# Kernel optimization log

Hardware: AMD Instinct MI355X
Metric: run time of the kernel (lower is better)

## Reference

```python
import jax, jax.numpy as jnp
import numpy as np

K = 50            # neighbors (self excluded)
ALPHA = 0.99      # propagation coefficient
THRESH = 0.4      # pseudo-label confidence threshold
MAXITER = 20      # CG iterations
NUM_CLASSES = 100
TOL = 1e-6        # CG relative tolerance (scipy cg tol)


def setup_inputs() -> dict:
    key = jax.random.key(0)
    k1, k2, k3 = jax.random.split(key, 3)
    N, d = 16384, 128
    X = jax.random.normal(k1, (N, d), dtype=jnp.float32)
    labels = jax.random.randint(k2, (N,), 0, NUM_CLASSES)
    labels_mask = jax.random.uniform(k3, (N,)) < 0.1
    idxs = jnp.arange(N)
    return {"X": X, "labels": labels, "labels_mask": labels_mask, "idxs": idxs}


def _label_prop(X, labels, labels_mask):
    N = X.shape[0]
    # faiss.normalize_L2 + inner-product search == cosine kNN
    Xn = X / jnp.maximum(jnp.linalg.norm(X, axis=1, keepdims=True), 1e-12)
    sims = Xn @ Xn.T                                   # [N, N]
    vals, I = jax.lax.top_k(sims, K + 1)
    Dv = vals[:, 1:] ** 3                              # drop self column, cube sims
    I = I[:, 1:]
    rows = jnp.repeat(jnp.arange(N), K)
    cols = I.reshape(-1)
    w = Dv.reshape(-1)
    # W = W + W.T with diagonal zeroed (edge-list form, never dense NxN)
    er = jnp.concatenate([rows, cols])
    ec = jnp.concatenate([cols, rows])
    ew = jnp.concatenate([w, w])
    ew = jnp.where(er == ec, 0.0, ew)
    S = jax.ops.segment_sum(ew, er, num_segments=N)
    S = jnp.where(S == 0, 1.0, S)
    Dinv = 1.0 / jnp.sqrt(S)                           # D^{-1/2}

    def A_mv(V):  # (I - alpha * D^-1/2 W D^-1/2) @ V, V: [N, C]
        U = Dinv[:, None] * V
        WU = jax.ops.segment_sum(ew[:, None] * U[ec], er, num_segments=N)
        return V - ALPHA * (Dinv[:, None] * WU)

    # per-class normalized seed vectors y (1/|labeled_c| on labeled idx of class c)
    mask_f = labels_mask.astype(jnp.float32)
    counts = jax.ops.segment_sum(mask_f, labels, num_segments=NUM_CLASSES)
    Y = (mask_f[:, None] * jax.nn.one_hot(labels, NUM_CLASSES, dtype=jnp.float32)) / jnp.maximum(counts, 1.0)[None, :]

    # batched CG (x0 = 0), all classes solved simultaneously; per-column early-stop mask
    bnorm = jnp.linalg.norm(Y, axis=0)
    x = jnp.zeros_like(Y)
    r = Y
    p = r
    rs = jnp.sum(r * r, axis=0)

    def step(carry, _):
        x, r, p, rs = carry
        active = jnp.sqrt(rs) > TOL * jnp.maximum(bnorm, 1e-30)
        Ap = A_mv(p)
        a = rs / jnp.maximum(jnp.sum(p * Ap, axis=0), 1e-30)
        a = jnp.where(active, a, 0.0)
        x = x + a * p
        r = r - a * Ap
        rs_new = jnp.sum(r * r, axis=0)
        beta = jnp.where(active, rs_new / jnp.maximum(rs, 1e-30), 0.0)
        p = jnp.where(active, r + beta * p, p)
        rs = jnp.where(active, rs_new, rs)
        return (x, r, p, rs), None

    (x, _, _, _), _ = jax.lax.scan(step, (x, r, p, rs), None, length=MAXITER)

    Z = jnp.maximum(x, 0.0)
    # torch F.normalize(Z, p=1, dim=1)
    probs_l1 = Z / jnp.maximum(jnp.sum(Z, axis=1, keepdims=True), 1e-12)
    pseudo = jax.nn.softmax(probs_l1, axis=-1)
    return pseudo


def reference(X, labels, labels_mask, idxs):
    pseudo = _label_prop(X, labels, labels_mask)
    max_probs = jnp.max(pseudo, axis=-1)
    p_labels = jnp.argmax(pseudo, axis=-1)
    masks = (max_probs >= THRESH).astype(jnp.float32)
    acc = jnp.mean((p_labels == labels).astype(jnp.float32))
    p_labels = jnp.where(labels_mask, labels, p_labels)  # overwrite labeled idx
    return p_labels, acc, masks
```

## Files before the change

### kernel.cpp

```cpp
#include <hip/hip_runtime.h>
#include <hip/hip_bf16.h>
#include <math.h>


#define N_NODES 16384
#define DIM     128
#define KNN     50
#define NCLS    100
#define PSTR    100
#define ALPHA_C 0.99f
#define TOL_C   1e-6f
#define TAU     0.18f
#define MAXITER_C 20

__global__ __launch_bounds__(256) void k_norm(const float* __restrict__ X, float* __restrict__ Xn){
  int t = threadIdx.x;
  int row = blockIdx.x*2 + (t>>7);
  int c = t & 127;
  float v = X[(size_t)row*DIM + c];
  float s = v*v;
  #pragma unroll
  for (int o=1;o<64;o<<=1) s += __shfl_xor(s, o, 64);
  __shared__ float sw[4];
  if ((t&63)==0) sw[t>>6] = s;
  __syncthreads();
  int half = (t>>7)*2;
  float nrm = fmaxf(sqrtf(sw[half]+sw[half+1]), 1e-12f);
  Xn[(size_t)row*DIM + c] = v / nrm;
}

#define NTILE 8256
__global__ __launch_bounds__(256, 4) void k_sims(const float* __restrict__ Xn,
    int* __restrict__ cand_cnt, float* __restrict__ cand_val, int* __restrict__ cand_idx, int CAP){
  __shared__ __align__(16) float As[32][132];
  __shared__ __align__(16) float Bs[32][132];
  const int t = threadIdx.x;
  const int tr = t >> 4, tc = t & 15;
  for (int q = blockIdx.x; q < NTILE; q += gridDim.x){
    float disc = 66049.0f - 8.0f*(float)q;
    int rb = (int)((257.0f - sqrtf(disc))*0.5f);
    if (rb > 127) rb = 127;
    while (rb > 0 && rb*(257-rb)/2 > q) --rb;
    while ((rb+1)*(257-(rb+1))/2 <= q) ++rb;
    int cb = rb + (q - rb*(257-rb)/2);
    const int row0 = rb*128, col0 = cb*128;
    float acc[8][8];
    #pragma unroll
    for (int i=0;i<8;i++){
      #pragma unroll
      for (int j=0;j<8;j++) acc[i][j]=0.f;
    }
    #pragma unroll 1
    for (int h=0; h<4; ++h){
      const int koff = h*32;
      __syncthreads();
      for (int v=t; v<1024; v+=256){
        int r = v>>3, k4 = (v&7)*4;
        float4 f = *(const float4*)(Xn + (size_t)(row0+r)*DIM + koff + k4);
        As[k4+0][r]=f.x; As[k4+1][r]=f.y; As[k4+2][r]=f.z; As[k4+3][r]=f.w;
        float4 g = *(const float4*)(Xn + (size_t)(col0+r)*DIM + koff + k4);
        Bs[k4+0][r]=g.x; Bs[k4+1][r]=g.y; Bs[k4+2][r]=g.z; Bs[k4+3][r]=g.w;
      }
      __syncthreads();
      #pragma unroll 4
      for (int k=0;k<32;k++){
        float a[8], b[8];
        *(float4*)&a[0] = *(const float4*)&As[k][tr*4];
        *(float4*)&a[4] = *(const float4*)&As[k][64+tr*4];
        *(float4*)&b[0] = *(const float4*)&Bs[k][tc*4];
        *(float4*)&b[4] = *(const float4*)&Bs[k][64+tc*4];
        #pragma unroll
        for (int i=0;i<8;i++){
          #pragma unroll
          for (int j=0;j<8;j++) acc[i][j] = fmaf(a[i], b[j], acc[i][j]);
        }
      }
    }
    #pragma unroll
    for (int i=0;i<8;i++){
      int row = row0 + ((i<4) ? (tr*4+i) : (64+tr*4+i-4));
      #pragma unroll
      for (int j=0;j<8;j++){
        float v = acc[i][j];
        if (v > TAU){
          int col = col0 + ((j<4) ? (tc*4+j) : (64+tc*4+j-4));
          if (rb == cb){
            if (col != row){
              int pos = atomicAdd(&cand_cnt[row], 1);
              if (pos < CAP){ size_t o=(size_t)row*CAP+pos; cand_val[o]=v; cand_idx[o]=col; }
            }
          } else {
            int pos = atomicAdd(&cand_cnt[row], 1);
            if (pos < CAP){ size_t o=(size_t)row*CAP+pos; cand_val[o]=v; cand_idx[o]=col; }
            int pos2 = atomicAdd(&cand_cnt[col], 1);
            if (pos2 < CAP){ size_t o=(size_t)col*CAP+pos2; cand_val[o]=v; cand_idx[o]=row; }
          }
        }
      }
    }
  }
}

__global__ __launch_bounds__(256) void k_select(const float* __restrict__ cand_val,
    const int* __restrict__ cand_idx, const int* __restrict__ cand_cnt, int CAP,
    int* __restrict__ nbr_idx, float* __restrict__ nbr_w, int* __restrict__ flags){
  int row = blockIdx.x; int t = threadIdx.x;
  int cnt = cand_cnt[row];
  if (cnt < KNN || cnt > CAP || cnt > 1024){ if (t==0) flags[row] = 1; return; }
  __shared__ unsigned long long sk[1024];
  int N = (cnt <= 512) ? 512 : 1024;
  for (int v=t; v<N; v+=256){
    unsigned long long key = 0ull;
    if (v < cnt){
      size_t o = (size_t)row*CAP + v;
      unsigned int fb = __float_as_uint(cand_val[o]);
      unsigned int ii = ~(unsigned int)cand_idx[o];
      key = ((unsigned long long)fb << 32) | (unsigned long long)ii;
    }
    sk[v] = key;
  }
  __syncthreads();
  for (int k=2; k<=N; k<<=1){
    for (int j=k>>1; j>0; j>>=1){
      for (int i=t; i<N; i+=256){
        int l = i ^ j;
        if (l > i){
          unsigned long long a = sk[i], b = sk[l];
          bool desc = ((i & k) == 0);
          bool sw = desc ? (a < b) : (a > b);
          if (sw){ sk[i] = b; sk[l] = a; }
        }
      }
      __syncthreads();
    }
  }
  if (t < KNN){
    unsigned long long key = sk[t];
    float v = __uint_as_float((unsigned int)(key >> 32));
    int ii = (int)(~(unsigned int)key);
    nbr_idx[(size_t)row*KNN + t] = ii;
    nbr_w[(size_t)row*KNN + t] = v*v*v;
  }
}

__global__ __launch_bounds__(256) void k_fallback(const float* __restrict__ Xn, const int* __restrict__ flags,
    int* __restrict__ nbr_idx, float* __restrict__ nbr_w){
  int row = blockIdx.x;
  if (flags[row]==0) return;
  int t = threadIdx.x;
  __shared__ float a[DIM];
  __shared__ float cv[256]; __shared__ int ci[256];
  __shared__ float bv[KNN]; __shared__ int bi[KNN];
  __shared__ int nf; __shared__ float minv; __shared__ int mini, minpos;
  if (t < DIM) a[t] = Xn[(size_t)row*DIM + t];
  if (t==0){ nf=0; minv=1e30f; mini=-1; minpos=-1; }
  __syncthreads();
  for (int c0=0; c0<N_NODES; c0+=256){
    int col = c0 + t;
    const float* xb = Xn + (size_t)col*DIM;
    float dot = 0.f;
    for (int k=0;k<DIM;k++) dot = fmaf(a[k], xb[k], dot);
    cv[t] = (col==row) ? -1e30f : dot;
    ci[t] = col;
    __syncthreads();
    if (t==0){
      for (int u=0; u<256; u++){
        float v = cv[u]; int ix = ci[u];
        if (v <= -1e29f) continue;
        if (nf < KNN){
          bv[nf]=v; bi[nf]=ix; nf++;
          if (nf==KNN){
            minpos=0; minv=bv[0]; mini=bi[0];
            for (int q=1;q<KNN;q++) if (bv[q]<minv || (bv[q]==minv && bi[q]>mini)){minv=bv[q];mini=bi[q];minpos=q;}
          }
        } else if (v>minv || (v==minv && ix<mini)){
          bv[minpos]=v; bi[minpos]=ix;
          minpos=0; minv=bv[0]; mini=bi[0];
          for (int q=1;q<KNN;q++) if (bv[q]<minv || (bv[q]==minv && bi[q]>mini)){minv=bv[q];mini=bi[q];minpos=q;}
        }
      }
    }
    __syncthreads();
  }
  if (t==0){
    for (int aa=1; aa<KNN; aa++){
      float kv=bv[aa]; int ki=bi[aa]; int b=aa-1;
      while (b>=0 && (bv[b]<kv || (bv[b]==kv && bi[b]>ki))){ bv[b+1]=bv[b]; bi[b+1]=bi[b]; b--; }
      bv[b+1]=kv; bi[b+1]=ki;
    }
    for (int q=0;q<KNN;q++){ nbr_idx[(size_t)row*KNN+q]=bi[q]; float v=bv[q]; nbr_w[(size_t)row*KNN+q]=v*v*v; }
  }
}

__global__ void k_indeg(const int* __restrict__ nbr_idx, int* __restrict__ indeg){
  int e = blockIdx.x*blockDim.x + threadIdx.x;
  if (e < N_NODES*KNN) atomicAdd(&indeg[nbr_idx[e]], 1);
}
__global__ __launch_bounds__(256) void k_scan(const int* __restrict__ indeg, int* __restrict__ offs){
  int t = threadIdx.x;
  __shared__ int ps[256];
  int base = t*64, s = 0;
  for (int m=0;m<64;m++) s += indeg[base+m];
  ps[t] = s; __syncthreads();
  if (t==0){ int run=0; for (int i=0;i<256;i++){ int tmp=ps[i]; ps[i]=run; run+=tmp; } offs[N_NODES]=run; }
  __syncthreads();
  int run = ps[t];
  for (int m=0;m<64;m++){ offs[base+m]=run; run += indeg[base+m]; }
}
__global__ void k_fill(const int* __restrict__ nbr_idx, const float* __restrict__ nbr_w,
    const int* __restrict__ offs, int* __restrict__ fillc, int* __restrict__ rev_src, float* __restrict__ rev_w){
  int e = blockIdx.x*blockDim.x + threadIdx.x;
  if (e >= N_NODES*KNN) return;
  int i = e / KNN;
  int j = nbr_idx[e];
  int pos = offs[j] + atomicAdd(&fillc[j], 1);
  rev_src[pos] = i;
  rev_w[pos]  = nbr_w[e];
}
__global__ __launch_bounds__(256) void k_sortrev(const int* __restrict__ offs, int* __restrict__ rev_src, float* __restrict__ rev_w){
  __shared__ int   ssrc[4][512];
  __shared__ float swv [4][512];
  int w = threadIdx.x>>6, lane = threadIdx.x&63;
  int node = blockIdx.x*4 + w;
  int e0 = offs[node], e1 = offs[node+1];
  int len = e1 - e0;
  if (len <= 1 || len > 512) return;
  for (int q=lane; q<len; q+=64){ ssrc[w][q]=rev_src[e0+q]; swv[w][q]=rev_w[e0+q]; }
  if (lane==0){
    for (int a=1;a<len;a++){
      int ks=ssrc[w][a]; float kw=swv[w][a]; int b=a-1;
      while (b>=0 && ssrc[w][b]>ks){ ssrc[w][b+1]=ssrc[w][b]; swv[w][b+1]=swv[w][b]; b--; }
      ssrc[w][b+1]=ks; swv[w][b+1]=kw;
    }
  }
  for (int q=lane; q<len; q+=64){ rev_src[e0+q]=ssrc[w][q]; rev_w[e0+q]=swv[w][q]; }
}
__global__ void k_degree(const float* __restrict__ nbr_w, const int* __restrict__ offs,
    const float* __restrict__ rev_w, float* __restrict__ Dinv){
  int i = blockIdx.x*blockDim.x + threadIdx.x;
  if (i >= N_NODES) return;
  float s = 0.f;
  for (int k=0;k<KNN;k++) s += nbr_w[(size_t)i*KNN+k];
  int e0=offs[i], e1=offs[i+1];
  for (int e=e0;e<e1;e++) s += rev_w[e];
  if (s == 0.f) s = 1.f;
  Dinv[i] = 1.0f / sqrtf(s);
}
__global__ void k_normw_fwd(const int* __restrict__ nbr_idx, float* __restrict__ nbr_w, const float* __restrict__ Dinv){
  int e = blockIdx.x*blockDim.x + threadIdx.x;
  if (e >= N_NODES*KNN) return;
  int i = e / KNN; int j = nbr_idx[e];
  nbr_w[e] *= Dinv[i]*Dinv[j];
}
__global__ __launch_bounds__(256) void k_normw_rev(const int* __restrict__ offs, const int* __restrict__ rev_src,
    float* __restrict__ rev_w, const float* __restrict__ Dinv){
  int wid = (blockIdx.x*256 + threadIdx.x)>>6; int lane = threadIdx.x&63;
  if (wid >= N_NODES) return;
  float di = Dinv[wid];
  int e1 = offs[wid+1];
  for (int e=offs[wid]+lane; e<e1; e+=64) rev_w[e] *= di*Dinv[rev_src[e]];
}

__global__ void k_clscnt(const int* __restrict__ labels, const int* __restrict__ mask, int* __restrict__ cls_cnt){
  int n = blockIdx.x*blockDim.x + threadIdx.x;
  if (n < N_NODES && mask[n]) atomicAdd(&cls_cnt[labels[n]], 1);
}
__global__ void k_init(const int* __restrict__ labels, const int* __restrict__ mask, const int* __restrict__ cls_cnt,
    float* __restrict__ x, float* __restrict__ r, float* __restrict__ p){
  int idx = blockIdx.x*blockDim.x + threadIdx.x;
  if (idx >= N_NODES*PSTR) return;
  int n = idx / PSTR, c = idx - n*PSTR;
  float y = 0.f;
  if (mask[n] && labels[n]==c) y = 1.0f / fmaxf((float)cls_cnt[c], 1.0f);
  x[idx]=0.f; r[idx]=y; p[idx]=y;
}

__global__ __launch_bounds__(256) void k_spmv_pap(const float* __restrict__ p, float* __restrict__ Ap,
    const int* __restrict__ nbr_idx, const float* __restrict__ nbr_w,
    const int* __restrict__ offs, const int* __restrict__ rev_src, const float* __restrict__ rev_w,
    float* __restrict__ part){
  int w = threadIdx.x>>6, l = threadIdx.x&63;
  int wid = blockIdx.x*4 + w;
  __shared__ float sh[4][100];
  if (l < 50){
    float accx=0.f, accy=0.f;
    const size_t base = (size_t)wid*KNN;
    for (int k=0;k<KNN;k++){
      int j = nbr_idx[base+k];
      float wv = nbr_w[base+k];
      float2 v = ((const float2*)(p + (size_t)j*PSTR))[l];
      accx = fmaf(wv, v.x, accx);
      accy = fmaf(wv, v.y, accy);
    }
    int e1 = offs[wid+1];
    for (int e=offs[wid]; e<e1; ++e){
      int j = rev_src[e];
      float wv = rev_w[e];
      float2 v = ((const float2*)(p + (size_t)j*PSTR))[l];
      accx = fmaf(wv, v.x, accx);
      accy = fmaf(wv, v.y, accy);
    }
    size_t o = (size_t)wid*PSTR;
    float2 pv = ((const float2*)(p + o))[l];
    float ax = pv.x - ALPHA_C*accx;
    float ay = pv.y - ALPHA_C*accy;
    ((float2*)(Ap + o))[l] = make_float2(ax, ay);
    sh[w][2*l]   = pv.x*ax;
    sh[w][2*l+1] = pv.y*ay;
  }
  __syncthreads();
  int tt = threadIdx.x;
  if (tt < 100) part[(size_t)blockIdx.x*100 + tt] = (sh[0][tt]+sh[1][tt]) + (sh[2][tt]+sh[3][tt]);
}
__global__ __launch_bounds__(256) void k_alpha(const float* __restrict__ part, const float* __restrict__ rs_cur,
    const float* __restrict__ bnorm, float* __restrict__ avec, int* __restrict__ actvec){
  int c = blockIdx.x, t = threadIdx.x;
  float s = 0.f;
  for (int b=t; b<4096; b+=256) s += part[(size_t)b*100 + c];
  #pragma unroll
  for (int o=1;o<64;o<<=1) s += __shfl_xor(s, o, 64);
  __shared__ float red[4];
  if ((t&63)==0) red[t>>6] = s;
  __syncthreads();
  if (t==0){
    float tot = (red[0]+red[1]) + (red[2]+red[3]);
    float rc = rs_cur[c];
    int act = sqrtf(rc) > TOL_C*fmaxf(bnorm[c], 1e-30f);
    avec[c] = act ? rc/fmaxf(tot, 1e-30f) : 0.f;
    actvec[c] = act;
  }
}
__global__ __launch_bounds__(256) void k_update_xr(float* __restrict__ x, float* __restrict__ r,
    const float* __restrict__ p, const float* __restrict__ Ap,
    const float* __restrict__ avec, float* __restrict__ part){
  int w = threadIdx.x>>6, l = threadIdx.x&63;
  int n = blockIdx.x*4 + w;
  __shared__ float sh[4][100];
  if (l < 50){
    size_t o = (size_t)n*PSTR;
    float2 av  = ((const float2*)avec)[l];
    float2 pv  = ((const float2*)(p + o))[l];
    float2 apv = ((const float2*)(Ap + o))[l];
    float2 xv  = ((const float2*)(x + o))[l];
    float2 rv  = ((const float2*)(r + o))[l];
    xv.x = fmaf(av.x, pv.x, xv.x);
    xv.y = fmaf(av.y, pv.y, xv.y);
    rv.x = rv.x - av.x*apv.x;
    rv.y = rv.y - av.y*apv.y;
    ((float2*)(x + o))[l] = xv;
    ((float2*)(r + o))[l] = rv;
    sh[w][2*l]   = rv.x*rv.x;
    sh[w][2*l+1] = rv.y*rv.y;
  }
  __syncthreads();
  int tt = threadIdx.x;
  if (tt < 100) part[(size_t)blockIdx.x*100 + tt] = (sh[0][tt]+sh[1][tt]) + (sh[2][tt]+sh[3][tt]);
}
__global__ __launch_bounds__(256) void k_beta(const float* __restrict__ part, const float* __restrict__ rs_cur,
    const int* __restrict__ actvec, float* __restrict__ rs_next, float* __restrict__ betavec){
  int c = blockIdx.x, t = threadIdx.x;
  float s = 0.f;
  for (int b=t; b<4096; b+=256) s += part[(size_t)b*100 + c];
  #pragma unroll
  for (int o=1;o<64;o<<=1) s += __shfl_xor(s, o, 64);
  __shared__ float red[4];
  if ((t&63)==0) red[t>>6] = s;
  __syncthreads();
  if (t==0){
    float tot = (red[0]+red[1]) + (red[2]+red[3]);
    float rc = rs_cur[c];
    int act = actvec[c];
    rs_next[c] = act ? tot : rc;
    betavec[c] = act ? tot/fmaxf(rc, 1e-30f) : 0.f;
  }
}
__global__ __launch_bounds__(256) void k_update_p(float* __restrict__ p, const float* __restrict__ r,
    const int* __restrict__ actvec, const float* __restrict__ betavec){
  int w = threadIdx.x>>6, l = threadIdx.x&63;
  int n = blockIdx.x*4 + w;
  if (l >= 50) return;
  size_t o = (size_t)n*PSTR;
  float2 bv = ((const float2*)betavec)[l];
  int2   av = ((const int2*)actvec)[l];
  float2 pv = ((const float2*)(p + o))[l];
  float2 rv = ((const float2*)(r + o))[l];
  pv.x = av.x ? fmaf(bv.x, pv.x, rv.x) : pv.x;
  pv.y = av.y ? fmaf(bv.y, pv.y, rv.y) : pv.y;
  ((float2*)(p + o))[l] = pv;
}
__global__ __launch_bounds__(256) void k_coldot0(const float* __restrict__ r, float* __restrict__ part){
  int w = threadIdx.x>>6, l = threadIdx.x&63;
  int n = blockIdx.x*4 + w;
  __shared__ float sh[4][100];
  if (l < 50){
    float2 rv = ((const float2*)(r + (size_t)n*PSTR))[l];
    sh[w][2*l]   = rv.x*rv.x;
    sh[w][2*l+1] = rv.y*rv.y;
  }
  __syncthreads();
  int tt = threadIdx.x;
  if (tt < 100) part[(size_t)blockIdx.x*100 + tt] = (sh[0][tt]+sh[1][tt]) + (sh[2][tt]+sh[3][tt]);
}
__global__ __launch_bounds__(256) void k_rs0(const float* __restrict__ part, float* __restrict__ rs0, float* __restrict__ bnorm){
  int c = blockIdx.x, t = threadIdx.x;
  float s = 0.f;
  for (int b=t; b<4096; b+=256) s += part[(size_t)b*100 + c];
  #pragma unroll
  for (int o=1;o<64;o<<=1) s += __shfl_xor(s, o, 64);
  __shared__ float red[4];
  if ((t&63)==0) red[t>>6] = s;
  __syncthreads();
  if (t==0){
    float tot = (red[0]+red[1]) + (red[2]+red[3]);
    rs0[c] = tot;
    bnorm[c] = sqrtf(tot);
  }
}

__global__ __launch_bounds__(256) void k_final(const float* __restrict__ x, const int* __restrict__ labels,
    const int* __restrict__ mask, float* __restrict__ out, int* __restrict__ acc_cnt){
  int n = blockIdx.x*blockDim.x + threadIdx.x;
  if (n >= N_NODES) return;
  const float* xr = x + (size_t)n*PSTR;
  float best = xr[0]; int arg = 0;
  for (int c=1;c<NCLS;c++){ float v = xr[c]; if (v > best){ best = v; arg = c; } }
  int plab = (best > 0.f) ? arg : 0;
  if (plab == labels[n]) atomicAdd(acc_cnt, 1);
  int lab = mask[n] ? labels[n] : plab;
  out[n] = (float)lab;
  out[N_NODES + 1 + n] = 0.f;
}
__global__ void k_acc(const int* __restrict__ acc_cnt, float* __restrict__ out){
  out[N_NODES] = (float)(*acc_cnt) / (float)N_NODES;
}

extern "C" void kernel_launch(void* const* d_in, const int* in_sizes, int n_in,
                              void* d_out, int out_size, void* d_ws, size_t ws_size,
                              hipStream_t stream){
  (void)in_sizes; (void)n_in; (void)out_size;
  const float* X      = (const float*)d_in[0];
  const int*   labels = (const int*)  d_in[1];
  const int*   mask   = (const int*)  d_in[2];
  float* out = (float*)d_out;

  char* ws = (char*)d_ws;
  size_t off = 0;
  auto alloc = [&](size_t bytes)->char*{ char* pp = ws + off; off += (bytes + 255) & ~(size_t)255; return pp; };

  float* Xn      = (float*)alloc((size_t)N_NODES*DIM*4);
  int*   nbr_idx = (int*)  alloc((size_t)N_NODES*KNN*4);
  float* nbr_w   = (float*)alloc((size_t)N_NODES*KNN*4);
  int*   indeg   = (int*)  alloc((size_t)N_NODES*4);
  int*   offs    = (int*)  alloc((size_t)(N_NODES+1)*4);
  int*   fillc   = (int*)  alloc((size_t)N_NODES*4);
  int*   rev_src = (int*)  alloc((size_t)N_NODES*KNN*4);
  float* rev_w   = (float*)alloc((size_t)N_NODES*KNN*4);
  float* Dinv    = (float*)alloc((size_t)N_NODES*4);
  int*   cls_cnt = (int*)  alloc(128*4);
  float* x  = (float*)alloc((size_t)N_NODES*PSTR*4);
  float* r  = (float*)alloc((size_t)N_NODES*PSTR*4);
  float* p  = (float*)alloc((size_t)N_NODES*PSTR*4);
  float* Ap = (float*)alloc((size_t)N_NODES*PSTR*4);
  float* rs_a   = (float*)alloc(128*4);
  float* rs_b   = (float*)alloc(128*4);
  float* avec   = (float*)alloc(128*4);
  float* betavec= (float*)alloc(128*4);
  int*   actvec = (int*)  alloc(128*4);
  float* bnorm  = (float*)alloc(128*4);
  float* part   = (float*)alloc((size_t)4096*100*4);
  int*   acc_cnt= (int*)  alloc(256);
  int*   flags  = (int*)  alloc((size_t)N_NODES*4);
  int*   cand_cnt=(int*)  alloc((size_t)N_NODES*4);

  size_t rem = (ws_size > off) ? (ws_size - off) : 0;
  size_t capc = rem/((size_t)N_NODES*8);
  int CAP = (int)(capc < 1024 ? capc : 1024);
  float* cand_val = (float*)alloc((size_t)N_NODES*CAP*4);
  int*   cand_idx = (int*)  alloc((size_t)N_NODES*CAP*4);

  hipMemsetAsync(cand_cnt, 0, (size_t)N_NODES*4, stream);
  hipMemsetAsync(flags,    0, (size_t)N_NODES*4, stream);
  hipMemsetAsync(indeg,    0, (size_t)N_NODES*4, stream);
  hipMemsetAsync(fillc,    0, (size_t)N_NODES*4, stream);
  hipMemsetAsync(cls_cnt,  0, 128*4, stream);
  hipMemsetAsync(acc_cnt,  0, 4, stream);

  k_norm    <<<N_NODES/2, 256, 0, stream>>>(X, Xn);
  k_sims    <<<1024, 256, 0, stream>>>(Xn, cand_cnt, cand_val, cand_idx, CAP);
  k_select  <<<N_NODES, 256, 0, stream>>>(cand_val, cand_idx, cand_cnt, CAP, nbr_idx, nbr_w, flags);
  k_fallback<<<N_NODES, 256, 0, stream>>>(Xn, flags, nbr_idx, nbr_w);
  k_indeg   <<<3200, 256, 0, stream>>>(nbr_idx, indeg);
  k_scan    <<<1, 256, 0, stream>>>(indeg, offs);
  k_fill    <<<3200, 256, 0, stream>>>(nbr_idx, nbr_w, offs, fillc, rev_src, rev_w);
  k_sortrev <<<4096, 256, 0, stream>>>(offs, rev_src, rev_w);
  k_degree  <<<64, 256, 0, stream>>>(nbr_w, offs, rev_w, Dinv);
  k_normw_fwd<<<3200, 256, 0, stream>>>(nbr_idx, nbr_w, Dinv);
  k_normw_rev<<<4096, 256, 0, stream>>>(offs, rev_src, rev_w, Dinv);
  k_clscnt  <<<64, 256, 0, stream>>>(labels, mask, cls_cnt);
  k_init    <<<(N_NODES*PSTR+255)/256, 256, 0, stream>>>(labels, mask, cls_cnt, x, r, p);
  k_coldot0 <<<4096, 256, 0, stream>>>(r, part);
  k_rs0     <<<100, 256, 0, stream>>>(part, rs_a, bnorm);

  for (int it=0; it<MAXITER_C; ++it){
    float* rs_cur = (it&1) ? rs_b : rs_a;
    float* rs_nxt = (it&1) ? rs_a : rs_b;
    k_spmv_pap <<<4096, 256, 0, stream>>>(p, Ap, nbr_idx, nbr_w, offs, rev_src, rev_w, part);
    k_alpha    <<<100, 256, 0, stream>>>(part, rs_cur, bnorm, avec, actvec);
    k_update_xr<<<4096, 256, 0, stream>>>(x, r, p, Ap, avec, part);
    k_beta     <<<100, 256, 0, stream>>>(part, rs_cur, actvec, rs_nxt, betavec);
    k_update_p <<<4096, 256, 0, stream>>>(p, r, actvec, betavec);
  }

  k_final<<<64, 256, 0, stream>>>(x, labels, mask, out, acc_cnt);
  k_acc  <<<1, 1, 0, stream>>>(acc_cnt, out);
}
```

Baseline: 3.787 ms.

## Double-buffer similarity GEMM tiles and split SpMV forward/reverse edges across waves

```diff
diff --git a/kernel.cpp b/kernel.cpp
--- a/kernel.cpp
+++ b/kernel.cpp
@@ -32,10 +32,12 @@
 #define NTILE 8256
 __global__ __launch_bounds__(256, 4) void k_sims(const float* __restrict__ Xn,
     int* __restrict__ cand_cnt, float* __restrict__ cand_val, int* __restrict__ cand_idx, int CAP){
-  __shared__ __align__(16) float As[32][132];
-  __shared__ __align__(16) float Bs[32][132];
+  __shared__ __align__(16) float As[2][16][132];
+  __shared__ __align__(16) float Bs[2][16][132];
   const int t = threadIdx.x;
   const int tr = t >> 4, tc = t & 15;
+  const int sr = t >> 1;
+  const int cg = (t & 1) * 8;
   for (int q = blockIdx.x; q < NTILE; q += gridDim.x){
     float disc = 66049.0f - 8.0f*(float)q;
     int rb = (int)((257.0f - sqrtf(disc))*0.5f);
@@ -44,36 +46,58 @@
     while ((rb+1)*(257-(rb+1))/2 <= q) ++rb;
     int cb = rb + (q - rb*(257-rb)/2);
     const int row0 = rb*128, col0 = cb*128;
+    const float* rowA = Xn + (size_t)(row0 + sr)*DIM + cg;
+    const float* rowB = Xn + (size_t)(col0 + sr)*DIM + cg;
     float acc[8][8];
     #pragma unroll
     for (int i=0;i<8;i++){
       #pragma unroll
       for (int j=0;j<8;j++) acc[i][j]=0.f;
     }
+    __syncthreads();
+    {
+      float4 fa0 = *(const float4*)(rowA);
+      float4 fa1 = *(const float4*)(rowA + 4);
+      float4 fb0 = *(const float4*)(rowB);
+      float4 fb1 = *(const float4*)(rowB + 4);
+      As[0][cg+0][sr]=fa0.x; As[0][cg+1][sr]=fa0.y; As[0][cg+2][sr]=fa0.z; As[0][cg+3][sr]=fa0.w;
+      As[0][cg+4][sr]=fa1.x; As[0][cg+5][sr]=fa1.y; As[0][cg+6][sr]=fa1.z; As[0][cg+7][sr]=fa1.w;
+      Bs[0][cg+0][sr]=fb0.x; Bs[0][cg+1][sr]=fb0.y; Bs[0][cg+2][sr]=fb0.z; Bs[0][cg+3][sr]=fb0.w;
+      Bs[0][cg+4][sr]=fb1.x; Bs[0][cg+5][sr]=fb1.y; Bs[0][cg+6][sr]=fb1.z; Bs[0][cg+7][sr]=fb1.w;
+    }
+    __syncthreads();
     #pragma unroll 1
-    for (int h=0; h<4; ++h){
-      const int koff = h*32;
-      __syncthreads();
-      for (int v=t; v<1024; v+=256){
-        int r = v>>3, k4 = (v&7)*4;
-        float4 f = *(const float4*)(Xn + (size_t)(row0+r)*DIM + koff + k4);
-        As[k4+0][r]=f.x; As[k4+1][r]=f.y; As[k4+2][r]=f.z; As[k4+3][r]=f.w;
-        float4 g = *(const float4*)(Xn + (size_t)(col0+r)*DIM + koff + k4);
-        Bs[k4+0][r]=g.x; Bs[k4+1][r]=g.y; Bs[k4+2][r]=g.z; Bs[k4+3][r]=g.w;
-      }
-      __syncthreads();
-      #pragma unroll 4
-      for (int k=0;k<32;k++){
+    for (int h=0; h<8; ++h){
+      const int buf = h & 1;
+      float4 fa0, fa1, fb0, fb1;
+      if (h < 7){
+        const float* na = rowA + (h+1)*16;
+        const float* nb = rowB + (h+1)*16;
+        fa0 = *(const float4*)(na);
+        fa1 = *(const float4*)(na + 4);
+        fb0 = *(const float4*)(nb);
+        fb1 = *(const float4*)(nb + 4);
+      }
+      #pragma unroll
+      for (int k=0;k<16;k++){
         float a[8], b[8];
-        *(float4*)&a[0] = *(const float4*)&As[k][tr*4];
-        *(float4*)&a[4] = *(const float4*)&As[k][64+tr*4];
-        *(float4*)&b[0] = *(const float4*)&Bs[k][tc*4];
-        *(float4*)&b[4] = *(const float4*)&Bs[k][64+tc*4];
+        *(float4*)&a[0] = *(const float4*)&As[buf][k][tr*4];
+        *(float4*)&a[4] = *(const float4*)&As[buf][k][64+tr*4];
+        *(float4*)&b[0] = *(const float4*)&Bs[buf][k][tc*4];
+        *(float4*)&b[4] = *(const float4*)&Bs[buf][k][64+tc*4];
         #pragma unroll
         for (int i=0;i<8;i++){
           #pragma unroll
           for (int j=0;j<8;j++) acc[i][j] = fmaf(a[i], b[j], acc[i][j]);
         }
+      }
+      if (h < 7){
+        const int nb_ = buf ^ 1;
+        As[nb_][cg+0][sr]=fa0.x; As[nb_][cg+1][sr]=fa0.y; As[nb_][cg+2][sr]=fa0.z; As[nb_][cg+3][sr]=fa0.w;
+        As[nb_][cg+4][sr]=fa1.x; As[nb_][cg+5][sr]=fa1.y; As[nb_][cg+6][sr]=fa1.z; As[nb_][cg+7][sr]=fa1.w;
+        Bs[nb_][cg+0][sr]=fb0.x; Bs[nb_][cg+1][sr]=fb0.y; Bs[nb_][cg+2][sr]=fb0.z; Bs[nb_][cg+3][sr]=fb0.w;
+        Bs[nb_][cg+4][sr]=fb1.x; Bs[nb_][cg+5][sr]=fb1.y; Bs[nb_][cg+6][sr]=fb1.z; Bs[nb_][cg+7][sr]=fb1.w;
+        __syncthreads();
       }
     }
     #pragma unroll
@@ -279,44 +303,57 @@
     const int* __restrict__ nbr_idx, const float* __restrict__ nbr_w,
     const int* __restrict__ offs, const int* __restrict__ rev_src, const float* __restrict__ rev_w,
     float* __restrict__ part){
-  int w = threadIdx.x>>6, l = threadIdx.x&63;
-  int wid = blockIdx.x*4 + w;
+  int t = threadIdx.x;
+  int w = t>>6, l = t&63;
+  int node = __builtin_amdgcn_readfirstlane(blockIdx.x*2 + (w>>1));
+  int half = w & 1;
   __shared__ float sh[4][100];
+  __shared__ float sh2[2][100];
   if (l < 50){
     float accx=0.f, accy=0.f;
-    const size_t base = (size_t)wid*KNN;
-    for (int k=0;k<KNN;k++){
-      int j = nbr_idx[base+k];
-      float wv = nbr_w[base+k];
-      float2 v = ((const float2*)(p + (size_t)j*PSTR))[l];
-      accx = fmaf(wv, v.x, accx);
-      accy = fmaf(wv, v.y, accy);
-    }
-    int e1 = offs[wid+1];
-    for (int e=offs[wid]; e<e1; ++e){
-      int j = rev_src[e];
-      float wv = rev_w[e];
-      float2 v = ((const float2*)(p + (size_t)j*PSTR))[l];
-      accx = fmaf(wv, v.x, accx);
-      accy = fmaf(wv, v.y, accy);
-    }
-    size_t o = (size_t)wid*PSTR;
-    float2 pv = ((const float2*)(p + o))[l];
-    float ax = pv.x - ALPHA_C*accx;
-    float ay = pv.y - ALPHA_C*accy;
-    ((float2*)(Ap + o))[l] = make_float2(ax, ay);
-    sh[w][2*l]   = pv.x*ax;
-    sh[w][2*l+1] = pv.y*ay;
-  }
-  __syncthreads();
-  int tt = threadIdx.x;
-  if (tt < 100) part[(size_t)blockIdx.x*100 + tt] = (sh[0][tt]+sh[1][tt]) + (sh[2][tt]+sh[3][tt]);
-}
-__global__ __launch_bounds__(256) void k_alpha(const float* __restrict__ part, const float* __restrict__ rs_cur,
+    if (half == 0){
+      const size_t base = (size_t)node*KNN;
+      #pragma unroll
+      for (int k=0;k<KNN;k++){
+        int j = nbr_idx[base+k];
+        float wv = nbr_w[base+k];
+        float2 v = ((const float2*)(p + (size_t)j*PSTR))[l];
+        accx = fmaf(wv, v.x, accx);
+        accy = fmaf(wv, v.y, accy);
+      }
+    } else {
+      int e0 = offs[node], e1 = offs[node+1];
+      for (int e=e0; e<e1; ++e){
+        int j = rev_src[e];
+        float wv = rev_w[e];
+        float2 v = ((const float2*)(p + (size_t)j*PSTR))[l];
+        accx = fmaf(wv, v.x, accx);
+        accy = fmaf(wv, v.y, accy);
+      }
+    }
+    sh[w][2*l]   = accx;
+    sh[w][2*l+1] = accy;
+  }
+  __syncthreads();
+  if (t < 200){
+    int nl = (t >= 100) ? 1 : 0;
+    int c = t - nl*100;
+    float acc = sh[nl*2][c] + sh[nl*2+1][c];
+    size_t o = (size_t)(blockIdx.x*2 + nl)*PSTR + c;
+    float pv = p[o];
+    float ap = pv - ALPHA_C*acc;
+    Ap[o] = ap;
+    sh2[nl][c] = pv*ap;
+  }
+  __syncthreads();
+  if (t < 100) part[(size_t)blockIdx.x*100 + t] = sh2[0][t] + sh2[1][t];
+}
+__global__ __launch_bounds__(256) void k_alpha(const float* __restrict__ part, int npart,
+    const float* __restrict__ rs_cur,
     const float* __restrict__ bnorm, float* __restrict__ avec, int* __restrict__ actvec){
   int c = blockIdx.x, t = threadIdx.x;
   float s = 0.f;
-  for (int b=t; b<4096; b+=256) s += part[(size_t)b*100 + c];
+  for (int b=t; b<npart; b+=256) s += part[(size_t)b*100 + c];
   #pragma unroll
   for (int o=1;o<64;o<<=1) s += __shfl_xor(s, o, 64);
   __shared__ float red[4];
@@ -356,11 +393,12 @@
   int tt = threadIdx.x;
   if (tt < 100) part[(size_t)blockIdx.x*100 + tt] = (sh[0][tt]+sh[1][tt]) + (sh[2][tt]+sh[3][tt]);
 }
-__global__ __launch_bounds__(256) void k_beta(const float* __restrict__ part, const float* __restrict__ rs_cur,
+__global__ __launch_bounds__(256) void k_beta(const float* __restrict__ part, int npart,
+    const float* __restrict__ rs_cur,
     const int* __restrict__ actvec, float* __restrict__ rs_next, float* __restrict__ betavec){
   int c = blockIdx.x, t = threadIdx.x;
   float s = 0.f;
-  for (int b=t; b<4096; b+=256) s += part[(size_t)b*100 + c];
+  for (int b=t; b<npart; b+=256) s += part[(size_t)b*100 + c];
   #pragma unroll
   for (int o=1;o<64;o<<=1) s += __shfl_xor(s, o, 64);
   __shared__ float red[4];
@@ -467,7 +505,7 @@
   float* betavec= (float*)alloc(128*4);
   int*   actvec = (int*)  alloc(128*4);
   float* bnorm  = (float*)alloc(128*4);
-  float* part   = (float*)alloc((size_t)4096*100*4);
+  float* part   = (float*)alloc((size_t)8192*100*4);
   int*   acc_cnt= (int*)  alloc(256);
   int*   flags  = (int*)  alloc((size_t)N_NODES*4);
   int*   cand_cnt=(int*)  alloc((size_t)N_NODES*4);
@@ -504,10 +542,10 @@
   for (int it=0; it<MAXITER_C; ++it){
     float* rs_cur = (it&1) ? rs_b : rs_a;
     float* rs_nxt = (it&1) ? rs_a : rs_b;
-    k_spmv_pap <<<4096, 256, 0, stream>>>(p, Ap, nbr_idx, nbr_w, offs, rev_src, rev_w, part);
-    k_alpha    <<<100, 256, 0, stream>>>(part, rs_cur, bnorm, avec, actvec);
+    k_spmv_pap <<<8192, 256, 0, stream>>>(p, Ap, nbr_idx, nbr_w, offs, rev_src, rev_w, part);
+    k_alpha    <<<100, 256, 0, stream>>>(part, 8192, rs_cur, bnorm, avec, actvec);
     k_update_xr<<<4096, 256, 0, stream>>>(x, r, p, Ap, avec, part);
-    k_beta     <<<100, 256, 0, stream>>>(part, rs_cur, actvec, rs_nxt, betavec);
+    k_beta     <<<100, 256, 0, stream>>>(part, 4096, rs_cur, actvec, rs_nxt, betavec);
     k_update_p <<<4096, 256, 0, stream>>>(p, r, actvec, betavec);
   }
 
```

Result: slower. 9.841 ms (+159.9%).
